# Kernel optimization log

Measured on AMD Instinct MI355X. Metric: run time of the kernel, lower is better.

Reference implementation:

```python
import jax, jax.numpy as jnp
import numpy as np

ATOM_FDIM = 133
BOND_FDIM = 147
HIDDEN = 300
DEPTH = 3
N_ATOMS = 100000
N_BONDS = 200000
MAX_NB = 6
N_MOLS = 4000


def setup_inputs() -> dict:
    key = jax.random.key(0)
    ks = jax.random.split(key, 10)
    f_atoms = jax.random.normal(ks[0], (N_ATOMS, ATOM_FDIM), dtype=jnp.float32)
    f_bonds = jax.random.normal(ks[1], (N_BONDS, BOND_FDIM), dtype=jnp.float32)
    a2b = jax.random.randint(ks[2], (N_ATOMS, MAX_NB), 0, N_BONDS)
    b2a = jax.random.randint(ks[3], (N_BONDS,), 0, N_ATOMS)
    b2revb = jax.random.randint(ks[4], (N_BONDS,), 0, N_BONDS)
    atom2mol = jnp.sort(jax.random.randint(ks[5], (N_ATOMS,), 0, N_MOLS))
    s = 1.0 / np.sqrt(HIDDEN)
    W_i = jax.random.uniform(ks[6], (BOND_FDIM, HIDDEN), jnp.float32, -s, s)
    W_h = jax.random.uniform(ks[7], (HIDDEN, HIDDEN), jnp.float32, -s, s)
    W_o_w = jax.random.uniform(ks[8], (ATOM_FDIM + HIDDEN, HIDDEN), jnp.float32, -s, s)
    W_o_b = jax.random.uniform(ks[9], (HIDDEN,), jnp.float32, -s, s)
    return {"f_atoms": f_atoms, "f_bonds": f_bonds, "a2b": a2b, "b2a": b2a,
            "b2revb": b2revb, "atom2mol": atom2mol, "W_i": W_i, "W_h": W_h,
            "W_o_w": W_o_w, "W_o_b": W_o_b}


def reference(f_atoms, f_bonds, a2b, b2a, b2revb, atom2mol, W_i, W_h, W_o_w, W_o_b):
    # input = W_i(f_bonds); message = act(input)
    inp = f_bonds @ W_i                      # [n_bonds, hidden]
    message = jax.nn.relu(inp)
    for _ in range(DEPTH - 1):
        # gather neighbor bond messages per atom and sum: [n_atoms, max_nb, h] -> [n_atoms, h]
        a_message = message[a2b].sum(axis=1)
        rev_message = message[b2revb]        # [n_bonds, hidden]
        message = a_message[b2a] - rev_message
        message = jax.nn.relu(inp + message @ W_h)
    # final atom-level aggregation
    a_message = message[a2b].sum(axis=1)     # [n_atoms, hidden]
    a_input = jnp.concatenate([f_atoms, a_message], axis=1)
    atom_hiddens = jax.nn.relu(a_input @ W_o_w + W_o_b)
    # segment mean pooling over molecules
    sums = jax.ops.segment_sum(atom_hiddens, atom2mol, num_segments=N_MOLS)
    counts = jax.ops.segment_sum(jnp.ones((atom_hiddens.shape[0],), atom_hiddens.dtype),
                                 atom2mol, num_segments=N_MOLS)
    mol_vecs = sums / jnp.maximum(counts, 1.0)[:, None]  # zero vec for empty mols
    return mol_vecs
```

## Files before the change

kernel.cpp:

```cpp
#include <hip/hip_runtime.h>
#include <stdint.h>

#define ATOM_FDIM 133
#define BOND_FDIM 147
#define HIDDEN    300
#define N_ATOMS   100000
#define N_BONDS   200000
#define MAX_NB    6
#define N_MOLS    4000

#define KP_I 160
#define KP_H 320
#define KP_O 448
#define LDA  304
#define CPR  38

#define TM   128
#define ACH  8
#define BCH  20

typedef unsigned short u16;
typedef short bf16x8 __attribute__((ext_vector_type(8)));
typedef float f32x4 __attribute__((ext_vector_type(4)));

__device__ __forceinline__ u16 f2bu(float f) {
    unsigned u = __float_as_uint(f);
    u += 0x7FFFu + ((u >> 16) & 1u);
    return (u16)(u >> 16);
}
__device__ __forceinline__ float bu2f(u16 b) { return __uint_as_float(((unsigned)b) << 16); }

__device__ __forceinline__ uint4 relu_bf16x8(uint4 v) {
    union { uint4 u; u16 s[8]; } x, o;
    x.u = v;
    #pragma unroll
    for (int e = 0; e < 8; ++e) o.s[e] = (x.s[e] & 0x8000u) ? (u16)0 : x.s[e];
    return o.u;
}
__device__ __forceinline__ uint4 comb_bf16x8(uint4 vi, uint4 va, uint4 vy) {
    union { uint4 u; u16 s[8]; } xi, xa, xy, o;
    xi.u = vi; xa.u = va; xy.u = vy;
    #pragma unroll
    for (int e = 0; e < 8; ++e)
        o.s[e] = f2bu(fmaxf(bu2f(xi.s[e]) + bu2f(xa.s[e]) - bu2f(xy.s[e]), 0.f));
    return o.u;
}

#define AS1 __attribute__((address_space(1)))
#define AS3 __attribute__((address_space(3)))
__device__ __forceinline__ void gl_lds(const void* g, void* l) {
    __builtin_amdgcn_global_load_lds((const AS1 void*)g, (AS3 void*)l, 16, 0, 0);
}

template <int EPI>
__global__ __launch_bounds__(512, 2) void mm_k(
    const u16* __restrict__ A, int lda,
    const u16* __restrict__ Wp,
    const float* __restrict__ bias,
    u16* __restrict__ out0, int ldo0,
    int M, int NT)
{
    __shared__ __align__(16) u16 As[3][ACH * 512];
    __shared__ __align__(16) u16 Bs[3][BCH * 512];

    const int t    = threadIdx.x;
    const int lane = t & 63, wid = t >> 6;
    const int fl   = lane & 15, fh = lane >> 4;
    const int m0   = blockIdx.x * TM;
    const int wr   = wid >> 1, wc = wid & 1;

    int arow = m0 + wid * 16 + fl;
    if (arow > M - 1) arow = M - 1;
    const char* srcAp = (const char*)A + (size_t)arow * (size_t)lda * 2u + (size_t)(fh * 16);
    const char* WpC = (const char*)Wp;
    const int bbase = (wid < 4) ? 3 * wid : 12 + 2 * (wid - 4);
    const size_t srcB0 = (size_t)bbase * 1024u + (size_t)lane * 16u;

    f32x4 acc[2][10] = {};

#define STAGE_T(kt, buf) do {                                                    \
        const size_t kbB_ = (size_t)(kt) * (size_t)(BCH * 1024);                 \
        gl_lds(srcAp + (size_t)(kt) * 64u, (char*)As[buf] + wid * 1024);         \
        gl_lds(WpC + kbB_ + srcB0,        (char*)Bs[buf] + bbase * 1024);        \
        gl_lds(WpC + kbB_ + srcB0 + 1024, (char*)Bs[buf] + bbase * 1024 + 1024); \
        if (wid < 4)                                                             \
            gl_lds(WpC + kbB_ + srcB0 + 2048, (char*)Bs[buf] + bbase * 1024 + 2048); \
    } while (0)

#define GATE() do {                                                        \
        if (wid < 4) asm volatile("s_waitcnt vmcnt(4)" ::: "memory");      \
        else         asm volatile("s_waitcnt vmcnt(3)" ::: "memory");      \
    } while (0)

    STAGE_T(0, 0);
    STAGE_T(1, 1);
    GATE();
    __builtin_amdgcn_s_barrier();

    int cur = 0;
    for (int tt = 0; tt < NT; ++tt) {
        int w2 = tt + 2; if (w2 >= NT) w2 -= NT;
        const int nx1 = (cur < 2) ? cur + 1 : 0;
        const int nx2 = (nx1 < 2) ? nx1 + 1 : 0;
        const u16* as_c = As[cur];
        const u16* bs_c = Bs[cur];
        const size_t kbB = (size_t)w2 * (size_t)(BCH * 1024);

        bf16x8 af0, af1, bfv[10];
        af0 = *reinterpret_cast<const bf16x8*>(&as_c[(wr * 2 + 0) * 512 + lane * 8]);
        af1 = *reinterpret_cast<const bf16x8*>(&as_c[(wr * 2 + 1) * 512 + lane * 8]);
        #pragma unroll
        for (int n = 0; n < 5; ++n)
            bfv[n] = *reinterpret_cast<const bf16x8*>(&bs_c[(wc * 10 + n) * 512 + lane * 8]);
        gl_lds(srcAp + (size_t)w2 * 64u, (char*)As[nx2] + wid * 1024);
        gl_lds(WpC + kbB + srcB0, (char*)Bs[nx2] + bbase * 1024);
        __builtin_amdgcn_s_barrier();
        __builtin_amdgcn_s_setprio(1);
        #pragma unroll
        for (int n = 0; n < 5; ++n) {
            acc[0][n] = __builtin_amdgcn_mfma_f32_16x16x32_bf16(af0, bfv[n], acc[0][n], 0, 0, 0);
            acc[1][n] = __builtin_amdgcn_mfma_f32_16x16x32_bf16(af1, bfv[n], acc[1][n], 0, 0, 0);
        }
        __builtin_amdgcn_s_setprio(0);
        __builtin_amdgcn_s_barrier();

        #pragma unroll
        for (int n = 5; n < 10; ++n)
            bfv[n] = *reinterpret_cast<const bf16x8*>(&bs_c[(wc * 10 + n) * 512 + lane * 8]);
        gl_lds(WpC + kbB + srcB0 + 1024, (char*)Bs[nx2] + bbase * 1024 + 1024);
        if (wid < 4)
            gl_lds(WpC + kbB + srcB0 + 2048, (char*)Bs[nx2] + bbase * 1024 + 2048);
        GATE();
        __builtin_amdgcn_s_barrier();
        __builtin_amdgcn_s_setprio(1);
        #pragma unroll
        for (int n = 5; n < 10; ++n) {
            acc[0][n] = __builtin_amdgcn_mfma_f32_16x16x32_bf16(af0, bfv[n], acc[0][n], 0, 0, 0);
            acc[1][n] = __builtin_amdgcn_mfma_f32_16x16x32_bf16(af1, bfv[n], acc[1][n], 0, 0, 0);
        }
        __builtin_amdgcn_s_setprio(0);
        __builtin_amdgcn_s_barrier();
        cur = nx1;
    }
#undef STAGE_T
#undef GATE

    #pragma unroll
    for (int m = 0; m < 2; ++m) {
        #pragma unroll
        for (int r = 0; r < 4; ++r) {
            const int row = m0 + wr * 32 + m * 16 + fh * 4 + r;
            if (row >= M) continue;
            #pragma unroll
            for (int n = 0; n < 10; ++n) {
                const int col = wc * 160 + n * 16 + fl;
                if (col >= HIDDEN) continue;
                const float v = acc[m][n][r];
                if (EPI == 1) out0[(size_t)row * ldo0 + col] = f2bu(v);
                else          out0[(size_t)row * ldo0 + col] = f2bu(fmaxf(v + bias[col], 0.f));
            }
        }
    }
}

template <int AM>
__global__ __launch_bounds__(512, 2) void mmf_k(
    const u16* __restrict__ A, int lda,
    const u16* __restrict__ aYp,
    const u16* __restrict__ Yp,
    const int* __restrict__ b2a,
    const int* __restrict__ b2revb,
    const u16* __restrict__ Wp,
    u16* __restrict__ out0, int ldo0,
    int M, int NT)
{
    __shared__ __align__(16) u16 As[2][ACH * 512];
    __shared__ __align__(16) u16 Bs[3][BCH * 512];

    const int t    = threadIdx.x;
    const int lane = t & 63, wid = t >> 6;
    const int fl   = lane & 15, fh = lane >> 4;
    const int m0   = blockIdx.x * TM;
    const int wr   = wid >> 1, wc = wid & 1;

    int arow = m0 + wid * 16 + fl;
    if (arow > M - 1) arow = M - 1;
    const char* pI = (const char*)A + (size_t)arow * (size_t)lda * 2u + (size_t)(fh * 16);
    const char* pA = nullptr; const char* pY = nullptr;
    if constexpr (AM == 2) {
        const int ia = b2a[arow], ir = b2revb[arow];
        pA = (const char*)aYp + (size_t)ia * (LDA * 2) + (size_t)(fh * 16);
        pY = (const char*)Yp  + (size_t)ir * (LDA * 2) + (size_t)(fh * 16);
    }
    const char* WpC = (const char*)Wp;
    const int bbase = (wid < 4) ? 3 * wid : 12 + 2 * (wid - 4);
    const size_t srcB0 = (size_t)bbase * 1024u + (size_t)lane * 16u;

    f32x4 acc[2][10] = {};
    uint4 Xi, Xa, Xy, Yi, Ya, Yy;
    (void)Xa; (void)Xy; (void)Ya; (void)Yy;

    Xi = *reinterpret_cast<const uint4*>(pI);
    if constexpr (AM == 2) { Xa = *reinterpret_cast<const uint4*>(pA);
                             Xy = *reinterpret_cast<const uint4*>(pY); }
    gl_lds(WpC + srcB0, (char*)Bs[0] + bbase * 1024);
    gl_lds(WpC + srcB0 + 1024, (char*)Bs[0] + bbase * 1024 + 1024);
    if (wid < 4) gl_lds(WpC + srcB0 + 2048, (char*)Bs[0] + bbase * 1024 + 2048);
    Yi = *reinterpret_cast<const uint4*>(pI + 64);
    if constexpr (AM == 2) { Ya = *reinterpret_cast<const uint4*>(pA + 64);
                             Yy = *reinterpret_cast<const uint4*>(pY + 64); }
    {
        const size_t kb1 = (size_t)(BCH * 1024);
        gl_lds(WpC + kb1 + srcB0, (char*)Bs[1] + bbase * 1024);
        gl_lds(WpC + kb1 + srcB0 + 1024, (char*)Bs[1] + bbase * 1024 + 1024);
        if (wid < 4) gl_lds(WpC + kb1 + srcB0 + 2048, (char*)Bs[1] + bbase * 1024 + 2048);
    }
    if constexpr (AM == 2) {
        if (wid < 4) asm volatile("s_waitcnt vmcnt(9)" ::: "memory");
        else         asm volatile("s_waitcnt vmcnt(7)" ::: "memory");
    } else {
        if (wid < 4) asm volatile("s_waitcnt vmcnt(7)" ::: "memory");
        else         asm volatile("s_waitcnt vmcnt(5)" ::: "memory");
    }
    {
        uint4 w0;
        if constexpr (AM == 2) w0 = comb_bf16x8(Xi, Xa, Xy);
        else                   w0 = relu_bf16x8(Xi);
        *reinterpret_cast<uint4*>(&As[0][wid * 512 + lane * 8]) = w0;
    }
    if constexpr (AM == 2) {
        if (wid < 4) asm volatile("s_waitcnt vmcnt(6)" ::: "memory");
        else         asm volatile("s_waitcnt vmcnt(5)" ::: "memory");
    } else {
        if (wid < 4) asm volatile("s_waitcnt vmcnt(4)" ::: "memory");
        else         asm volatile("s_waitcnt vmcnt(3)" ::: "memory");
    }
    asm volatile("s_waitcnt lgkmcnt(0)" ::: "memory");
    __builtin_amdgcn_s_barrier();

    int tt = 0, bcur = 0;

#define GATE() do {                                                        \
    if constexpr (AM == 2) {                                               \
        if (wid < 4) asm volatile("s_waitcnt vmcnt(6)" ::: "memory");      \
        else         asm volatile("s_waitcnt vmcnt(5)" ::: "memory");      \
    } else {                                                               \
        if (wid < 4) asm volatile("s_waitcnt vmcnt(4)" ::: "memory");      \
        else         asm volatile("s_waitcnt vmcnt(3)" ::: "memory");      \
    } } while (0)

#define STEP(LI, LA, LY, WI, WA, WY) do {                                                   \
    int w2 = tt + 2; if (w2 >= NT) w2 -= NT;                                                \
    const u16* as_c = As[tt & 1];                                                           \
    const u16* bs_c = Bs[bcur];                                                             \
    int bnx = bcur + 2; if (bnx >= 3) bnx -= 3;                                             \
    char* bdst = (char*)Bs[bnx] + bbase * 1024;                                             \
    const size_t kbB = (size_t)w2 * (size_t)(BCH * 1024);                                   \
    bf16x8 af0, af1, bfv[10];                                                               \
    af0 = *reinterpret_cast<const bf16x8*>(&as_c[(wr * 2 + 0) * 512 + lane * 8]);           \
    af1 = *reinterpret_cast<const bf16x8*>(&as_c[(wr * 2 + 1) * 512 + lane * 8]);           \
    _Pragma("unroll")                                                                       \
    for (int n = 0; n < 5; ++n)                                                             \
        bfv[n] = *reinterpret_cast<const bf16x8*>(&bs_c[(wc * 10 + n) * 512 + lane * 8]);   \
    LI = *reinterpret_cast<const uint4*>(pI + (size_t)w2 * 64u);                            \
    if constexpr (AM == 2) {                                                                \
        LA = *reinterpret_cast<const uint4*>(pA + (size_t)w2 * 64u);                        \
        LY = *reinterpret_cast<const uint4*>(pY + (size_t)w2 * 64u);                        \
    }                                                                                       \
    gl_lds(WpC + kbB + srcB0, bdst);                                                        \
    __builtin_amdgcn_s_barrier();                                                           \
    __builtin_amdgcn_s_setprio(1);                                                          \
    _Pragma("unroll")                                                                       \
    for (int n = 0; n < 5; ++n) {                                                           \
        acc[0][n] = __builtin_amdgcn_mfma_f32_16x16x32_bf16(af0, bfv[n], acc[0][n], 0,0,0); \
        acc[1][n] = __builtin_amdgcn_mfma_f32_16x16x32_bf16(af1, bfv[n], acc[1][n], 0,0,0); \
    }                                                                                       \
    __builtin_amdgcn_s_setprio(0);                                                          \
    __builtin_amdgcn_s_barrier();                                                           \
    _Pragma("unroll")                                                                       \
    for (int n = 5; n < 10; ++n)                                                            \
        bfv[n] = *reinterpret_cast<const bf16x8*>(&bs_c[(wc * 10 + n) * 512 + lane * 8]);   \
    gl_lds(WpC + kbB + srcB0 + 1024, bdst + 1024);                                          \
    if (wid < 4) gl_lds(WpC + kbB + srcB0 + 2048, bdst + 2048);                             \
    GATE();                                                                                 \
    {                                                                                       \
        uint4 wv;                                                                           \
        if constexpr (AM == 2) wv = comb_bf16x8(WI, WA, WY);                                \
        else                   wv = relu_bf16x8(WI);                                        \
        *reinterpret_cast<uint4*>(&As[(tt + 1) & 1][wid * 512 + lane * 8]) = wv;            \
    }                                                                                       \
    asm volatile("s_waitcnt lgkmcnt(0)" ::: "memory");                                      \
    __builtin_amdgcn_s_barrier();                                                           \
    __builtin_amdgcn_s_setprio(1);                                                          \
    _Pragma("unroll")                                                                       \
    for (int n = 5; n < 10; ++n) {                                                          \
        acc[0][n] = __builtin_amdgcn_mfma_f32_16x16x32_bf16(af0, bfv[n], acc[0][n], 0,0,0); \
        acc[1][n] = __builtin_amdgcn_mfma_f32_16x16x32_bf16(af1, bfv[n], acc[1][n], 0,0,0); \
    }                                                                                       \
    __builtin_amdgcn_s_setprio(0);                                                          \
    __builtin_amdgcn_s_barrier();                                                           \
    ++tt; bcur = (bcur == 2) ? 0 : bcur + 1;                                                \
} while (0)

    while (tt + 1 < NT) {
        STEP(Xi, Xa, Xy, Yi, Ya, Yy);
        STEP(Yi, Ya, Yy, Xi, Xa, Xy);
    }
    if (tt < NT) STEP(Xi, Xa, Xy, Yi, Ya, Yy);
#undef STEP
#undef GATE

    #pragma unroll
    for (int m = 0; m < 2; ++m) {
        #pragma unroll
        for (int r = 0; r < 4; ++r) {
            const int row = m0 + wr * 32 + m * 16 + fh * 4 + r;
            if (row >= M) continue;
            #pragma unroll
            for (int n = 0; n < 10; ++n) {
                const int col = wc * 160 + n * 16 + fl;
                if (col >= HIDDEN) continue;
                out0[(size_t)row * ldo0 + col] = f2bu(acc[m][n][r]);
            }
        }
    }
}

__global__ __launch_bounds__(256) void wconv_k(const float* __restrict__ W,
                                               int split, int off1, int Ktot, int NT,
                                               u16* __restrict__ Wp)
{
    const int id = blockIdx.x * 256 + threadIdx.x;
    if (id >= NT * BCH * 512) return;
    const int block = id >> 9, rem = id & 511;
    const int l = rem >> 3, e = rem & 7;
    const int c = block % BCH, kt = block / BCH;
    const int col = c * 16 + (l & 15);
    const int k   = kt * 32 + (l >> 4) * 8 + e;
    float v = 0.f;
    if (col < HIDDEN) {
        if (k < split) {
            const int r = k + off1;
            if (r < Ktot) v = W[(size_t)r * HIDDEN + col];
        } else {
            const int r = k - split;
            if (r < off1) v = W[(size_t)r * HIDDEN + col];
        }
    }
    Wp[id] = f2bu(v);
}

__global__ __launch_bounds__(256) void fbconv_k(const float* __restrict__ fb, u16* __restrict__ dst)
{
    const int id = blockIdx.x * 256 + threadIdx.x;
    if (id >= N_BONDS * KP_I) return;
    const int r = id / KP_I, k = id - r * KP_I;
    dst[id] = f2bu(k < BOND_FDIM ? fb[(size_t)r * BOND_FDIM + k] : 0.f);
}

__global__ __launch_bounds__(256) void agg_k(const u16* __restrict__ src,
                                             const int* __restrict__ a2b,
                                             u16* __restrict__ dst)
{
    const int c = blockIdx.x * 256 + threadIdx.x;
    if (c >= N_ATOMS * CPR) return;
    const int a = c / CPR, q = c - a * CPR;
    const int h = q * 8;
    const int* nb = a2b + (size_t)a * MAX_NB;
    float s[8] = {};
    #pragma unroll
    for (int j = 0; j < MAX_NB; ++j) {
        const int r = nb[j];
        union { uint4 u; u16 s[8]; } x;
        x.u = *(const uint4*)(src + (size_t)r * LDA + h);
        #pragma unroll
        for (int e = 0; e < 8; ++e) s[e] += bu2f(x.s[e]);
    }
    union { uint4 u; u16 s[8]; } o;
    #pragma unroll
    for (int e = 0; e < 8; ++e) o.s[e] = f2bu(s[e]);
    *(uint4*)(dst + (size_t)a * LDA + h) = o.u;
}

__global__ __launch_bounds__(256) void comb_k(const u16* __restrict__ inp,
                                              const u16* __restrict__ aY,
                                              const u16* __restrict__ Y,
                                              const int* __restrict__ b2a,
                                              const int* __restrict__ b2revb,
                                              u16* __restrict__ msg)
{
    const int c = blockIdx.x * 256 + threadIdx.x;
    if (c >= N_BONDS * CPR) return;
    const int b = c / CPR, q = c - b * CPR;
    const int h = q * 8;
    const int ia = b2a[b], ir = b2revb[b];
    union { uint4 u; u16 s[8]; } xi, xa, xy, o;
    xi.u = *(const uint4*)(inp + (size_t)b * LDA + h);
    xa.u = *(const uint4*)(aY + (size_t)ia * LDA + h);
    xy.u = *(const uint4*)(Y + (size_t)ir * LDA + h);
    #pragma unroll
    for (int j = 0; j < 8; ++j)
        o.s[j] = f2bu(fmaxf(bu2f(xi.s[j]) + bu2f(xa.s[j]) - bu2f(xy.s[j]), 0.f));
    *(uint4*)(msg + (size_t)b * LDA + h) = o.u;
}

__global__ __launch_bounds__(256) void aggcat_k(const u16* __restrict__ msg,
                                                const int* __restrict__ a2b,
                                                const float* __restrict__ fa,
                                                u16* __restrict__ dst)
{
    const int id = blockIdx.x * 256 + threadIdx.x;
    if (id >= N_ATOMS * (KP_O / 4)) return;
    const int a = id / (KP_O / 4), c = id - a * (KP_O / 4);
    const int e0 = c * 4;
    union { uint2 u; u16 s[4]; } o;
    if (e0 < HIDDEN) {
        const int* nb = a2b + (size_t)a * MAX_NB;
        float s0 = 0.f, s1 = 0.f, s2 = 0.f, s3 = 0.f;
        #pragma unroll
        for (int j = 0; j < MAX_NB; ++j) {
            union { uint2 u; u16 s[4]; } x;
            x.u = *(const uint2*)(msg + (size_t)nb[j] * LDA + e0);
            s0 += bu2f(x.s[0]); s1 += bu2f(x.s[1]); s2 += bu2f(x.s[2]); s3 += bu2f(x.s[3]);
        }
        o.s[0] = f2bu(s0); o.s[1] = f2bu(s1); o.s[2] = f2bu(s2); o.s[3] = f2bu(s3);
    } else {
        #pragma unroll
        for (int j = 0; j < 4; ++j) {
            const int fi = e0 + j - HIDDEN;
            o.s[j] = (fi < ATOM_FDIM) ? f2bu(fa[(size_t)a * ATOM_FDIM + fi]) : (u16)0;
        }
    }
    *(uint2*)(dst + (size_t)a * KP_O + e0) = o.u;
}

__global__ __launch_bounds__(320) void pool_k(const u16* __restrict__ ah,
                                              const int* __restrict__ a2m,
                                              float* __restrict__ out)
{
    const int m = blockIdx.x;
    int lo, hi;
    { int l = 0, r = N_ATOMS;
      while (l < r) { int mid = (l + r) >> 1; if (a2m[mid] < m) l = mid + 1; else r = mid; }
      lo = l; }
    { int l = lo, r = N_ATOMS;
      while (l < r) { int mid = (l + r) >> 1; if (a2m[mid] < m + 1) l = mid + 1; else r = mid; }
      hi = l; }
    const float inv = 1.0f / (float)((hi - lo) > 1 ? (hi - lo) : 1);
    const int h = threadIdx.x;
    if (h >= HIDDEN) return;
    float s = 0.f;
    for (int a = lo; a < hi; ++a) s += bu2f(ah[(size_t)a * LDA + h]);
    out[(size_t)m * HIDDEN + h] = s * inv;
}

extern "C" void kernel_launch(void* const* d_in, const int* in_sizes, int n_in,
                              void* d_out, int out_size, void* d_ws, size_t ws_size,
                              hipStream_t stream)
{
    const float* f_atoms  = (const float*)d_in[0];
    const float* f_bonds  = (const float*)d_in[1];
    const int*   a2b      = (const int*)d_in[2];
    const int*   b2a      = (const int*)d_in[3];
    const int*   b2revb   = (const int*)d_in[4];
    const int*   atom2mol = (const int*)d_in[5];
    const float* W_i      = (const float*)d_in[6];
    const float* W_h      = (const float*)d_in[7];
    const float* W_o_w    = (const float*)d_in[8];
    const float* W_o_b    = (const float*)d_in[9];
    float* out = (float*)d_out;

    char* p = (char*)d_ws;
    auto alloc = [&](size_t bytes) { char* r = p; p += (bytes + 255) & ~(size_t)255; return r; };
    u16* B0 = (u16*)alloc(((size_t)N_BONDS + 16) * LDA * 2);
    u16* B1 = (u16*)alloc(((size_t)N_BONDS + 16) * LDA * 2);
    u16* B2 = (u16*)alloc(((size_t)N_BONDS + 16) * LDA * 2);
    u16* aY = (u16*)alloc(((size_t)N_ATOMS + 16) * LDA * 2);
    u16* Wpi = (u16*)alloc((size_t)(KP_I / 32) * BCH * 512 * 2);
    u16* Wph = (u16*)alloc((size_t)(KP_H / 32) * BCH * 512 * 2);
    u16* Wpo = (u16*)alloc((size_t)(KP_O / 32) * BCH * 512 * 2);
    if ((size_t)(p - (char*)d_ws) > ws_size) return;

    u16* inp    = B0;
    u16* fb16   = B1;
    u16* Y1     = B1;
    u16* Y2     = B2;
    u16* msg2   = B1;
    u16* concat = B2;
    u16* ah     = B0;

    const dim3 blk(256);
    auto g1 = [](long long n) { return dim3((unsigned)((n + 255) / 256)); };
    const dim3 blk5(512);
    const dim3 gB((N_BONDS + TM - 1) / TM);
    const dim3 gA((N_ATOMS + TM - 1) / TM);

    const int BIGSPLIT = 1 << 20;
    wconv_k<<<g1((long long)(KP_I / 32) * BCH * 512), blk, 0, stream>>>(
        W_i, BIGSPLIT, 0, BOND_FDIM, KP_I / 32, Wpi);
    wconv_k<<<g1((long long)(KP_H / 32) * BCH * 512), blk, 0, stream>>>(
        W_h, BIGSPLIT, 0, HIDDEN, KP_H / 32, Wph);
    wconv_k<<<g1((long long)(KP_O / 32) * BCH * 512), blk, 0, stream>>>(
        W_o_w, HIDDEN, ATOM_FDIM, ATOM_FDIM + HIDDEN, KP_O / 32, Wpo);
    fbconv_k<<<g1((long long)N_BONDS * KP_I), blk, 0, stream>>>(f_bonds, fb16);

    mm_k<1><<<gB, blk5, 0, stream>>>(fb16, KP_I, Wpi, nullptr,
                                     inp, LDA, N_BONDS, KP_I / 32);

    mmf_k<1><<<gB, blk5, 0, stream>>>(inp, LDA, nullptr, nullptr, nullptr, nullptr,
                                      Wph, Y1, LDA, N_BONDS, KP_H / 32);
    agg_k<<<g1((long long)N_ATOMS * CPR), blk, 0, stream>>>(Y1, a2b, aY);

    mmf_k<2><<<gB, blk5, 0, stream>>>(inp, LDA, aY, Y1, b2a, b2revb,
                                      Wph, Y2, LDA, N_BONDS, KP_H / 32);
    agg_k<<<g1((long long)N_ATOMS * CPR), blk, 0, stream>>>(Y2, a2b, aY);

    comb_k<<<g1((long long)N_BONDS * CPR), blk, 0, stream>>>(inp, aY, Y2, b2a, b2revb, msg2);
    aggcat_k<<<g1((long long)N_ATOMS * (KP_O / 4)), blk, 0, stream>>>(msg2, a2b, f_atoms, concat);

    mm_k<2><<<gA, blk5, 0, stream>>>(concat, KP_O, Wpo, W_o_b,
                                     ah, LDA, N_ATOMS, KP_O / 32);
    pool_k<<<dim3(N_MOLS), dim3(320), 0, stream>>>(ah, atom2mol, out);
}
```

Before: 840.1 us.

## Double K-tile depth to 64 per iteration in GEMM pipelines

```diff
diff --git a/kernel.cpp b/kernel.cpp
--- a/kernel.cpp
+++ b/kernel.cpp
@@ -9,14 +9,13 @@
 #define MAX_NB    6
 #define N_MOLS    4000
 
-#define KP_I 160
+#define KP_I 192
 #define KP_H 320
-#define KP_O 448
+#define KP_O 512
 #define LDA  304
 #define CPR  38
 
 #define TM   128
-#define ACH  8
 #define BCH  20
 
 typedef unsigned short u16;
@@ -51,6 +50,7 @@
 __device__ __forceinline__ void gl_lds(const void* g, void* l) {
     __builtin_amdgcn_global_load_lds((const AS1 void*)g, (AS3 void*)l, 16, 0, 0);
 }
+#define MFMA(a, b, c) __builtin_amdgcn_mfma_f32_16x16x32_bf16((a), (b), (c), 0, 0, 0)
 
 template <int EPI>
 __global__ __launch_bounds__(512, 2) void mm_k(
@@ -60,8 +60,8 @@
     u16* __restrict__ out0, int ldo0,
     int M, int NT)
 {
-    __shared__ __align__(16) u16 As[3][ACH * 512];
-    __shared__ __align__(16) u16 Bs[3][BCH * 512];
+    __shared__ __align__(16) u16 As[3][16 * 512];
+    __shared__ __align__(16) u16 Bs[2][40 * 512];
 
     const int t    = threadIdx.x;
     const int lane = t & 63, wid = t >> 6;
@@ -73,77 +73,74 @@
     if (arow > M - 1) arow = M - 1;
     const char* srcAp = (const char*)A + (size_t)arow * (size_t)lda * 2u + (size_t)(fh * 16);
     const char* WpC = (const char*)Wp;
-    const int bbase = (wid < 4) ? 3 * wid : 12 + 2 * (wid - 4);
-    const size_t srcB0 = (size_t)bbase * 1024u + (size_t)lane * 16u;
+    const size_t srcB0 = (size_t)(5 * wid) * 1024u + (size_t)lane * 16u;
 
     f32x4 acc[2][10] = {};
 
-#define STAGE_T(kt, buf) do {                                                    \
-        const size_t kbB_ = (size_t)(kt) * (size_t)(BCH * 1024);                 \
-        gl_lds(srcAp + (size_t)(kt) * 64u, (char*)As[buf] + wid * 1024);         \
-        gl_lds(WpC + kbB_ + srcB0,        (char*)Bs[buf] + bbase * 1024);        \
-        gl_lds(WpC + kbB_ + srcB0 + 1024, (char*)Bs[buf] + bbase * 1024 + 1024); \
-        if (wid < 4)                                                             \
-            gl_lds(WpC + kbB_ + srcB0 + 2048, (char*)Bs[buf] + bbase * 1024 + 2048); \
+#define STAGE_A(kt, buf) do {                                                      \
+        gl_lds(srcAp + (size_t)(kt) * 128u,      (char*)As[buf] + wid * 1024);     \
+        gl_lds(srcAp + (size_t)(kt) * 128u + 64, (char*)As[buf] + 8192 + wid * 1024); \
     } while (0)
-
-#define GATE() do {                                                        \
-        if (wid < 4) asm volatile("s_waitcnt vmcnt(4)" ::: "memory");      \
-        else         asm volatile("s_waitcnt vmcnt(3)" ::: "memory");      \
+#define STAGE_B(kt, buf) do {                                                      \
+        const size_t kb_ = (size_t)(kt) * 40960u;                                  \
+        _Pragma("unroll")                                                          \
+        for (int j = 0; j < 5; ++j)                                                \
+            gl_lds(WpC + kb_ + srcB0 + (size_t)j * 1024,                           \
+                   (char*)Bs[buf] + 5 * wid * 1024 + j * 1024);                    \
     } while (0)
 
-    STAGE_T(0, 0);
-    STAGE_T(1, 1);
-    GATE();
+    STAGE_A(0, 0);
+    STAGE_B(0, 0);
+    STAGE_A(1, 1);
+    asm volatile("s_waitcnt vmcnt(2)" ::: "memory");
     __builtin_amdgcn_s_barrier();
 
     int cur = 0;
     for (int tt = 0; tt < NT; ++tt) {
+        int w1 = tt + 1; if (w1 >= NT) w1 -= NT;
         int w2 = tt + 2; if (w2 >= NT) w2 -= NT;
         const int nx1 = (cur < 2) ? cur + 1 : 0;
         const int nx2 = (nx1 < 2) ? nx1 + 1 : 0;
         const u16* as_c = As[cur];
-        const u16* bs_c = Bs[cur];
-        const size_t kbB = (size_t)w2 * (size_t)(BCH * 1024);
+        const u16* bs_c = Bs[tt & 1];
 
         bf16x8 af0, af1, bfv[10];
         af0 = *reinterpret_cast<const bf16x8*>(&as_c[(wr * 2 + 0) * 512 + lane * 8]);
         af1 = *reinterpret_cast<const bf16x8*>(&as_c[(wr * 2 + 1) * 512 + lane * 8]);
         #pragma unroll
-        for (int n = 0; n < 5; ++n)
+        for (int n = 0; n < 10; ++n)
             bfv[n] = *reinterpret_cast<const bf16x8*>(&bs_c[(wc * 10 + n) * 512 + lane * 8]);
-        gl_lds(srcAp + (size_t)w2 * 64u, (char*)As[nx2] + wid * 1024);
-        gl_lds(WpC + kbB + srcB0, (char*)Bs[nx2] + bbase * 1024);
+        STAGE_B(w1, (tt + 1) & 1);
         __builtin_amdgcn_s_barrier();
         __builtin_amdgcn_s_setprio(1);
         #pragma unroll
-        for (int n = 0; n < 5; ++n) {
-            acc[0][n] = __builtin_amdgcn_mfma_f32_16x16x32_bf16(af0, bfv[n], acc[0][n], 0, 0, 0);
-            acc[1][n] = __builtin_amdgcn_mfma_f32_16x16x32_bf16(af1, bfv[n], acc[1][n], 0, 0, 0);
+        for (int n = 0; n < 10; ++n) {
+            acc[0][n] = MFMA(af0, bfv[n], acc[0][n]);
+            acc[1][n] = MFMA(af1, bfv[n], acc[1][n]);
         }
         __builtin_amdgcn_s_setprio(0);
         __builtin_amdgcn_s_barrier();
 
-        #pragma unroll
-        for (int n = 5; n < 10; ++n)
-            bfv[n] = *reinterpret_cast<const bf16x8*>(&bs_c[(wc * 10 + n) * 512 + lane * 8]);
-        gl_lds(WpC + kbB + srcB0 + 1024, (char*)Bs[nx2] + bbase * 1024 + 1024);
-        if (wid < 4)
-            gl_lds(WpC + kbB + srcB0 + 2048, (char*)Bs[nx2] + bbase * 1024 + 2048);
-        GATE();
+        af0 = *reinterpret_cast<const bf16x8*>(&as_c[(8 + wr * 2 + 0) * 512 + lane * 8]);
+        af1 = *reinterpret_cast<const bf16x8*>(&as_c[(8 + wr * 2 + 1) * 512 + lane * 8]);
+        #pragma unroll
+        for (int n = 0; n < 10; ++n)
+            bfv[n] = *reinterpret_cast<const bf16x8*>(&bs_c[(20 + wc * 10 + n) * 512 + lane * 8]);
+        STAGE_A(w2, nx2);
+        asm volatile("s_waitcnt vmcnt(2)" ::: "memory");
         __builtin_amdgcn_s_barrier();
         __builtin_amdgcn_s_setprio(1);
         #pragma unroll
-        for (int n = 5; n < 10; ++n) {
-            acc[0][n] = __builtin_amdgcn_mfma_f32_16x16x32_bf16(af0, bfv[n], acc[0][n], 0, 0, 0);
-            acc[1][n] = __builtin_amdgcn_mfma_f32_16x16x32_bf16(af1, bfv[n], acc[1][n], 0, 0, 0);
+        for (int n = 0; n < 10; ++n) {
+            acc[0][n] = MFMA(af0, bfv[n], acc[0][n]);
+            acc[1][n] = MFMA(af1, bfv[n], acc[1][n]);
         }
         __builtin_amdgcn_s_setprio(0);
         __builtin_amdgcn_s_barrier();
         cur = nx1;
     }
-#undef STAGE_T
-#undef GATE
+#undef STAGE_A
+#undef STAGE_B
 
     #pragma unroll
     for (int m = 0; m < 2; ++m) {
@@ -174,8 +171,8 @@
     u16* __restrict__ out0, int ldo0,
     int M, int NT)
 {
-    __shared__ __align__(16) u16 As[2][ACH * 512];
-    __shared__ __align__(16) u16 Bs[3][BCH * 512];
+    __shared__ __align__(16) u16 As[2][16 * 512];
+    __shared__ __align__(16) u16 Bs[2][40 * 512];
 
     const int t    = threadIdx.x;
     const int lane = t & 63, wid = t >> 6;
@@ -193,122 +190,103 @@
         pY = (const char*)Yp  + (size_t)ir * (LDA * 2) + (size_t)(fh * 16);
     }
     const char* WpC = (const char*)Wp;
-    const int bbase = (wid < 4) ? 3 * wid : 12 + 2 * (wid - 4);
-    const size_t srcB0 = (size_t)bbase * 1024u + (size_t)lane * 16u;
+    const size_t srcB0 = (size_t)(5 * wid) * 1024u + (size_t)lane * 16u;
 
     f32x4 acc[2][10] = {};
-    uint4 Xi, Xa, Xy, Yi, Ya, Yy;
-    (void)Xa; (void)Xy; (void)Ya; (void)Yy;
-
-    Xi = *reinterpret_cast<const uint4*>(pI);
-    if constexpr (AM == 2) { Xa = *reinterpret_cast<const uint4*>(pA);
-                             Xy = *reinterpret_cast<const uint4*>(pY); }
-    gl_lds(WpC + srcB0, (char*)Bs[0] + bbase * 1024);
-    gl_lds(WpC + srcB0 + 1024, (char*)Bs[0] + bbase * 1024 + 1024);
-    if (wid < 4) gl_lds(WpC + srcB0 + 2048, (char*)Bs[0] + bbase * 1024 + 2048);
-    Yi = *reinterpret_cast<const uint4*>(pI + 64);
-    if constexpr (AM == 2) { Ya = *reinterpret_cast<const uint4*>(pA + 64);
-                             Yy = *reinterpret_cast<const uint4*>(pY + 64); }
-    {
-        const size_t kb1 = (size_t)(BCH * 1024);
-        gl_lds(WpC + kb1 + srcB0, (char*)Bs[1] + bbase * 1024);
-        gl_lds(WpC + kb1 + srcB0 + 1024, (char*)Bs[1] + bbase * 1024 + 1024);
-        if (wid < 4) gl_lds(WpC + kb1 + srcB0 + 2048, (char*)Bs[1] + bbase * 1024 + 2048);
-    }
-    if constexpr (AM == 2) {
-        if (wid < 4) asm volatile("s_waitcnt vmcnt(9)" ::: "memory");
-        else         asm volatile("s_waitcnt vmcnt(7)" ::: "memory");
-    } else {
-        if (wid < 4) asm volatile("s_waitcnt vmcnt(7)" ::: "memory");
-        else         asm volatile("s_waitcnt vmcnt(5)" ::: "memory");
-    }
-    {
-        uint4 w0;
-        if constexpr (AM == 2) w0 = comb_bf16x8(Xi, Xa, Xy);
-        else                   w0 = relu_bf16x8(Xi);
-        *reinterpret_cast<uint4*>(&As[0][wid * 512 + lane * 8]) = w0;
-    }
-    if constexpr (AM == 2) {
-        if (wid < 4) asm volatile("s_waitcnt vmcnt(6)" ::: "memory");
-        else         asm volatile("s_waitcnt vmcnt(5)" ::: "memory");
-    } else {
-        if (wid < 4) asm volatile("s_waitcnt vmcnt(4)" ::: "memory");
-        else         asm volatile("s_waitcnt vmcnt(3)" ::: "memory");
-    }
+    uint4 Xi0, Xi1, Xa0, Xa1, Xy0, Xy1;
+    uint4 Yi0, Yi1, Ya0, Ya1, Yy0, Yy1;
+    (void)Xa0; (void)Xa1; (void)Xy0; (void)Xy1;
+    (void)Ya0; (void)Ya1; (void)Yy0; (void)Yy1;
+
+#define STAGE_B(kt, buf) do {                                                      \
+        const size_t kb_ = (size_t)(kt) * 40960u;                                  \
+        _Pragma("unroll")                                                          \
+        for (int j = 0; j < 5; ++j)                                                \
+            gl_lds(WpC + kb_ + srcB0 + (size_t)j * 1024,                           \
+                   (char*)Bs[buf] + 5 * wid * 1024 + j * 1024);                    \
+    } while (0)
+#define LOADSET(kt, I0, I1, A0, A1, Y0, Y1) do {                                   \
+        const size_t kb_ = (size_t)(kt) * 128u;                                    \
+        I0 = *reinterpret_cast<const uint4*>(pI + kb_);                            \
+        I1 = *reinterpret_cast<const uint4*>(pI + kb_ + 64);                       \
+        if constexpr (AM == 2) {                                                   \
+            A0 = *reinterpret_cast<const uint4*>(pA + kb_);                        \
+            A1 = *reinterpret_cast<const uint4*>(pA + kb_ + 64);                   \
+            Y0 = *reinterpret_cast<const uint4*>(pY + kb_);                        \
+            Y1 = *reinterpret_cast<const uint4*>(pY + kb_ + 64);                   \
+        }                                                                          \
+    } while (0)
+#define XF(I, Aa, Yy) (AM == 2 ? comb_bf16x8(I, Aa, Yy) : relu_bf16x8(I))
+
+    LOADSET(0, Xi0, Xi1, Xa0, Xa1, Xy0, Xy1);
+    STAGE_B(0, 0);
+    LOADSET(1, Yi0, Yi1, Ya0, Ya1, Yy0, Yy1);
+    if constexpr (AM == 2) asm volatile("s_waitcnt vmcnt(11)" ::: "memory");
+    else                   asm volatile("s_waitcnt vmcnt(7)"  ::: "memory");
+    *reinterpret_cast<uint4*>(&As[0][wid * 512 + lane * 8])       = XF(Xi0, Xa0, Xy0);
+    *reinterpret_cast<uint4*>(&As[0][(8 + wid) * 512 + lane * 8]) = XF(Xi1, Xa1, Xy1);
+    if constexpr (AM == 2) asm volatile("s_waitcnt vmcnt(6)" ::: "memory");
+    else                   asm volatile("s_waitcnt vmcnt(2)" ::: "memory");
     asm volatile("s_waitcnt lgkmcnt(0)" ::: "memory");
     __builtin_amdgcn_s_barrier();
 
-    int tt = 0, bcur = 0;
-
-#define GATE() do {                                                        \
-    if constexpr (AM == 2) {                                               \
-        if (wid < 4) asm volatile("s_waitcnt vmcnt(6)" ::: "memory");      \
-        else         asm volatile("s_waitcnt vmcnt(5)" ::: "memory");      \
-    } else {                                                               \
-        if (wid < 4) asm volatile("s_waitcnt vmcnt(4)" ::: "memory");      \
-        else         asm volatile("s_waitcnt vmcnt(3)" ::: "memory");      \
-    } } while (0)
-
-#define STEP(LI, LA, LY, WI, WA, WY) do {                                                   \
+    int tt = 0;
+
+#define STEP(LI0, LI1, LA0, LA1, LY0, LY1, WI0, WI1, WA0, WA1, WY0, WY1) do {               \
+    int w1 = tt + 1; if (w1 >= NT) w1 -= NT;                                                \
     int w2 = tt + 2; if (w2 >= NT) w2 -= NT;                                                \
     const u16* as_c = As[tt & 1];                                                           \
-    const u16* bs_c = Bs[bcur];                                                             \
-    int bnx = bcur + 2; if (bnx >= 3) bnx -= 3;                                             \
-    char* bdst = (char*)Bs[bnx] + bbase * 1024;                                             \
-    const size_t kbB = (size_t)w2 * (size_t)(BCH * 1024);                                   \
+    const u16* bs_c = Bs[tt & 1];                                                           \
     bf16x8 af0, af1, bfv[10];                                                               \
+                                                                     \
     af0 = *reinterpret_cast<const bf16x8*>(&as_c[(wr * 2 + 0) * 512 + lane * 8]);           \
     af1 = *reinterpret_cast<const bf16x8*>(&as_c[(wr * 2 + 1) * 512 + lane * 8]);           \
     _Pragma("unroll")                                                                       \
-    for (int n = 0; n < 5; ++n)                                                             \
+    for (int n = 0; n < 10; ++n)                                                            \
         bfv[n] = *reinterpret_cast<const bf16x8*>(&bs_c[(wc * 10 + n) * 512 + lane * 8]);   \
-    LI = *reinterpret_cast<const uint4*>(pI + (size_t)w2 * 64u);                            \
-    if constexpr (AM == 2) {                                                                \
-        LA = *reinterpret_cast<const uint4*>(pA + (size_t)w2 * 64u);                        \
-        LY = *reinterpret_cast<const uint4*>(pY + (size_t)w2 * 64u);                        \
-    }                                                                                       \
-    gl_lds(WpC + kbB + srcB0, bdst);                                                        \
+    STAGE_B(w1, (tt + 1) & 1);                                        \
+    LOADSET(w2, LI0, LI1, LA0, LA1, LY0, LY1);                                              \
     __builtin_amdgcn_s_barrier();                                                           \
     __builtin_amdgcn_s_setprio(1);                                                          \
     _Pragma("unroll")                                                                       \
-    for (int n = 0; n < 5; ++n) {                                                           \
-        acc[0][n] = __builtin_amdgcn_mfma_f32_16x16x32_bf16(af0, bfv[n], acc[0][n], 0,0,0); \
-        acc[1][n] = __builtin_amdgcn_mfma_f32_16x16x32_bf16(af1, bfv[n], acc[1][n], 0,0,0); \
+    for (int n = 0; n < 10; ++n) {                                                          \
+        acc[0][n] = MFMA(af0, bfv[n], acc[0][n]);                                           \
+        acc[1][n] = MFMA(af1, bfv[n], acc[1][n]);                                           \
     }                                                                                       \
     __builtin_amdgcn_s_setprio(0);                                                          \
     __builtin_amdgcn_s_barrier();                                                           \
+                                                                     \
+    af0 = *reinterpret_cast<const bf16x8*>(&as_c[(8 + wr * 2 + 0) * 512 + lane * 8]);       \
+    af1 = *reinterpret_cast<const bf16x8*>(&as_c[(8 + wr * 2 + 1) * 512 + lane * 8]);       \
     _Pragma("unroll")                                                                       \
-    for (int n = 5; n < 10; ++n)                                                            \
-        bfv[n] = *reinterpret_cast<const bf16x8*>(&bs_c[(wc * 10 + n) * 512 + lane * 8]);   \
-    gl_lds(WpC + kbB + srcB0 + 1024, bdst + 1024);                                          \
-    if (wid < 4) gl_lds(WpC + kbB + srcB0 + 2048, bdst + 2048);                             \
-    GATE();                                                                                 \
-    {                                                                                       \
-        uint4 wv;                                                                           \
-        if constexpr (AM == 2) wv = comb_bf16x8(WI, WA, WY);                                \
-        else                   wv = relu_bf16x8(WI);                                        \
-        *reinterpret_cast<uint4*>(&As[(tt + 1) & 1][wid * 512 + lane * 8]) = wv;            \
-    }                                                                                       \
+    for (int n = 0; n < 10; ++n)                                                            \
+        bfv[n] = *reinterpret_cast<const bf16x8*>(&bs_c[(20 + wc * 10 + n) * 512 + lane * 8]); \
+    if constexpr (AM == 2) asm volatile("s_waitcnt vmcnt(6)" ::: "memory");                 \
+    else                   asm volatile("s_waitcnt vmcnt(2)" ::: "memory");                 \
+    *reinterpret_cast<uint4*>(&As[(tt + 1) & 1][wid * 512 + lane * 8])       = XF(WI0, WA0, WY0); \
+    *reinterpret_cast<uint4*>(&As[(tt + 1) & 1][(8 + wid) * 512 + lane * 8]) = XF(WI1, WA1, WY1); \
     asm volatile("s_waitcnt lgkmcnt(0)" ::: "memory");                                      \
     __builtin_amdgcn_s_barrier();                                                           \
     __builtin_amdgcn_s_setprio(1);                                                          \
     _Pragma("unroll")                                                                       \
-    for (int n = 5; n < 10; ++n) {                                                          \
-        acc[0][n] = __builtin_amdgcn_mfma_f32_16x16x32_bf16(af0, bfv[n], acc[0][n], 0,0,0); \
-        acc[1][n] = __builtin_amdgcn_mfma_f32_16x16x32_bf16(af1, bfv[n], acc[1][n], 0,0,0); \
+    for (int n = 0; n < 10; ++n) {                                                          \
+        acc[0][n] = MFMA(af0, bfv[n], acc[0][n]);                                           \
+        acc[1][n] = MFMA(af1, bfv[n], acc[1][n]);                                           \
     }                                                                                       \
     __builtin_amdgcn_s_setprio(0);                                                          \
     __builtin_amdgcn_s_barrier();                                                           \
-    ++tt; bcur = (bcur == 2) ? 0 : bcur + 1;                                                \
+    ++tt;                                                                                   \
 } while (0)
 
     while (tt + 1 < NT) {
-        STEP(Xi, Xa, Xy, Yi, Ya, Yy);
-        STEP(Yi, Ya, Yy, Xi, Xa, Xy);
-    }
-    if (tt < NT) STEP(Xi, Xa, Xy, Yi, Ya, Yy);
+        STEP(Xi0, Xi1, Xa0, Xa1, Xy0, Xy1, Yi0, Yi1, Ya0, Ya1, Yy0, Yy1);
+        STEP(Yi0, Yi1, Ya0, Ya1, Yy0, Yy1, Xi0, Xi1, Xa0, Xa1, Xy0, Xy1);
+    }
+    if (tt < NT) STEP(Xi0, Xi1, Xa0, Xa1, Xy0, Xy1, Yi0, Yi1, Ya0, Ya1, Yy0, Yy1);
 #undef STEP
-#undef GATE
+#undef LOADSET
+#undef STAGE_B
+#undef XF
 
     #pragma unroll
     for (int m = 0; m < 2; ++m) {
@@ -327,11 +305,11 @@
 }
 
 __global__ __launch_bounds__(256) void wconv_k(const float* __restrict__ W,
-                                               int split, int off1, int Ktot, int NT,
+                                               int split, int off1, int Ktot, int NT32,
                                                u16* __restrict__ Wp)
 {
     const int id = blockIdx.x * 256 + threadIdx.x;
-    if (id >= NT * BCH * 512) return;
+    if (id >= NT32 * BCH * 512) return;
     const int block = id >> 9, rem = id & 511;
     const int l = rem >> 3, e = rem & 7;
     const int c = block % BCH, kt = block / BCH;
@@ -428,7 +406,7 @@
         #pragma unroll
         for (int j = 0; j < 4; ++j) {
             const int fi = e0 + j - HIDDEN;
-            o.s[j] = (fi < ATOM_FDIM) ? f2bu(fa[(size_t)a * ATOM_FDIM + fi]) : (u16)0;
+            o.s[j] = (fi >= 0 && fi < ATOM_FDIM) ? f2bu(fa[(size_t)a * ATOM_FDIM + fi]) : (u16)0;
         }
     }
     *(uint2*)(dst + (size_t)a * KP_O + e0) = o.u;
@@ -505,20 +483,20 @@
     fbconv_k<<<g1((long long)N_BONDS * KP_I), blk, 0, stream>>>(f_bonds, fb16);
 
     mm_k<1><<<gB, blk5, 0, stream>>>(fb16, KP_I, Wpi, nullptr,
-                                     inp, LDA, N_BONDS, KP_I / 32);
+                                     inp, LDA, N_BONDS, KP_I / 64);
 
     mmf_k<1><<<gB, blk5, 0, stream>>>(inp, LDA, nullptr, nullptr, nullptr, nullptr,
-                                      Wph, Y1, LDA, N_BONDS, KP_H / 32);
+                                      Wph, Y1, LDA, N_BONDS, KP_H / 64);
     agg_k<<<g1((long long)N_ATOMS * CPR), blk, 0, stream>>>(Y1, a2b, aY);
 
     mmf_k<2><<<gB, blk5, 0, stream>>>(inp, LDA, aY, Y1, b2a, b2revb,
-                                      Wph, Y2, LDA, N_BONDS, KP_H / 32);
+                                      Wph, Y2, LDA, N_BONDS, KP_H / 64);
     agg_k<<<g1((long long)N_ATOMS * CPR), blk, 0, stream>>>(Y2, a2b, aY);
 
     comb_k<<<g1((long long)N_BONDS * CPR), blk, 0, stream>>>(inp, aY, Y2, b2a, b2revb, msg2);
     aggcat_k<<<g1((long long)N_ATOMS * (KP_O / 4)), blk, 0, stream>>>(msg2, a2b, f_atoms, concat);
 
     mm_k<2><<<gA, blk5, 0, stream>>>(concat, KP_O, Wpo, W_o_b,
-                                     ah, LDA, N_ATOMS, KP_O / 32);
+                                     ah, LDA, N_ATOMS, KP_O / 64);
     pool_k<<<dim3(N_MOLS), dim3(320), 0, stream>>>(ah, atom2mol, out);
 }
```

Measured after the change: 849.3 us. About the same (+1.1%).
